# Kernel optimization log

Hardware: AMD Instinct MI355X
Metric: run time of the kernel (lower is better)

Reference implementation:

```python
import jax, jax.numpy as jnp
import numpy as np

N = 50000      # n_nodes
E = 1600000    # n_edges (avg degree 32)
IN = 512       # in_channels
H = 64         # hidden_channels
L = 32         # latent_channels


def _glorot(key, shape):
    lim = np.sqrt(6.0 / (shape[0] + shape[1])).astype(np.float32)
    return jax.random.uniform(key, shape, jnp.float32, -lim, lim)


def setup_inputs() -> dict:
    key = jax.random.key(0)
    ks = jax.random.split(key, 8)
    return {
        "x": jax.random.normal(ks[0], (N, IN), jnp.float32),
        "edge_index": jax.random.randint(ks[1], (2, E), 0, N, dtype=jnp.int64),
        "W1": _glorot(ks[2], (IN, H)), "b1": jnp.zeros((H,), jnp.float32),
        "W2": _glorot(ks[3], (H, L)), "b2": jnp.zeros((L,), jnp.float32),
        "Wd1": _glorot(ks[4], (L, H)), "bd1": jnp.zeros((H,), jnp.float32),
        "Wd2": _glorot(ks[5], (H, IN)), "bd2": jnp.zeros((IN,), jnp.float32),
    }


def reference(x, edge_index, W1, b1, W2, b2, Wd1, bd1, Wd2, bd2):
    n = x.shape[0]
    # GCNConv: add self-loops, symmetric normalization D^-1/2 (A+I) D^-1/2
    loops = jnp.arange(n, dtype=edge_index.dtype)
    src = jnp.concatenate([edge_index[0], loops])  # message sources
    dst = jnp.concatenate([edge_index[1], loops])  # aggregation targets
    deg = jax.ops.segment_sum(jnp.ones(src.shape[0], jnp.float32), dst,
                              num_segments=n)      # deg >= 1 (self-loop)
    dis = jax.lax.rsqrt(deg)                       # deg_inv_sqrt
    norm = dis[src] * dis[dst]                     # [E+N] edge coefficients

    def gcn_conv(h, W, b):
        hw = h @ W                                 # linear first (thin GEMM)
        msg = hw[src] * norm[:, None]              # gather + scale
        return jax.ops.segment_sum(msg, dst, num_segments=n) + b

    h = jax.nn.relu(gcn_conv(x, W1, b1))
    z = jax.nn.relu(gcn_conv(h, W2, b2))
    d = jax.nn.relu(z @ Wd1 + bd1)
    return jax.nn.sigmoid(d @ Wd2 + bd2)
```

## Files before the change

kernel.cpp:

```cpp
#include <hip/hip_runtime.h>

#define NN 50000
#define NE 1600000
#define CIN 512
#define CH 64
#define CL 32

#define SCAN_CHUNK 1024
#define NSCAN ((NN + SCAN_CHUNK - 1) / SCAN_CHUNK)

#define BKN 256
#define NB ((NN + BKN - 1) / BKN)
#define CHUNK 8192
#define NBLKA ((NE + CHUNK - 1) / CHUNK)
#define SEGCAP 12288

typedef float f32x4 __attribute__((ext_vector_type(4)));
typedef short bf16x8 __attribute__((ext_vector_type(8)));


__device__ inline unsigned short bf_hi(float f) {
    union { float f; unsigned u; } a; a.f = f;
    unsigned r = a.u + 0x7FFFu + ((a.u >> 16) & 1u);
    return (unsigned short)(r >> 16);
}
__device__ inline float bf_to_f(unsigned short h) {
    union { unsigned u; float f; } b; b.u = ((unsigned)h) << 16; return b.f;
}
__device__ inline void split_bf16(float f, unsigned short& hi, unsigned short& lo) {
    hi = bf_hi(f);
    lo = bf_hi(f - bf_to_f(hi));
}
__device__ inline void split4(const float4& v, ushort4& h, ushort4& l) {
    split_bf16(v.x, h.x, l.x); split_bf16(v.y, h.y, l.y);
    split_bf16(v.z, h.z, l.z); split_bf16(v.w, h.w, l.w);
}
__device__ inline void split8(const float4& v0, const float4& v1, bf16x8& h, bf16x8& l) {
    ushort4 h0, l0, h1, l1;
    split4(v0, h0, l0); split4(v1, h1, l1);
    h = (bf16x8){(short)h0.x, (short)h0.y, (short)h0.z, (short)h0.w,
                 (short)h1.x, (short)h1.y, (short)h1.z, (short)h1.w};
    l = (bf16x8){(short)l0.x, (short)l0.y, (short)l0.z, (short)l0.w,
                 (short)l1.x, (short)l1.y, (short)l1.z, (short)l1.w};
}

__device__ inline bf16x8 frag(const char* plane, int row, int koff_bytes) {
    int off = (row * 128 + koff_bytes) ^ ((row & 7) << 4);
    return *(const bf16x8*)(plane + off);
}


__global__ void k_prep(const float* __restrict__ W1, const float* __restrict__ Wd2,
                       unsigned short* __restrict__ wt1_hi, unsigned short* __restrict__ wt1_lo,
                       unsigned short* __restrict__ wt2_hi, unsigned short* __restrict__ wt2_lo) {
    int id = blockIdx.x * blockDim.x + threadIdx.x;
    if (id < CIN * CH) {
        int k = id >> 6, n = id & 63;
        unsigned short h, lo; split_bf16(W1[id], h, lo);
        wt1_hi[n * CIN + k] = h; wt1_lo[n * CIN + k] = lo;
    } else {
        int e = id - CIN * CH;
        int k = e >> 9, n = e & 511;
        unsigned short h, lo; split_bf16(Wd2[e], h, lo);
        wt2_hi[n * CH + k] = h; wt2_lo[n * CH + k] = lo;
    }
}


__global__ void k_init(int* cnt, int* gcur) {
    int i = blockIdx.x * blockDim.x + threadIdx.x;
    if (i < NN) cnt[i] = 0;
    if (i < NB) gcur[i] = 0;
}

__global__ void k_deg(const int* __restrict__ dst, int* __restrict__ cnt) {
    int e = blockIdx.x * blockDim.x + threadIdx.x;
    if (e < NE) atomicAdd(&cnt[dst[e]], 1);
}

__global__ void k_dis(const int* __restrict__ cnt, float* __restrict__ dis) {
    int i = blockIdx.x * blockDim.x + threadIdx.x;
    if (i < NN) dis[i] = rsqrtf((float)(cnt[i] + 1));
}

__global__ void k_scan_block(const int* __restrict__ cnt, int* __restrict__ rowptr,
                             int* __restrict__ bsum) {
    __shared__ int sd[256];
    int t = threadIdx.x, b = blockIdx.x;
    int base = b * SCAN_CHUNK + t * 4;
    int c[4], s = 0;
#pragma unroll
    for (int j = 0; j < 4; j++) {
        int i = base + j;
        c[j] = (i < NN) ? cnt[i] : 0;
        s += c[j];
    }
    sd[t] = s;
    __syncthreads();
    for (int off = 1; off < 256; off <<= 1) {
        int v = (t >= off) ? sd[t - off] : 0;
        __syncthreads();
        sd[t] += v;
        __syncthreads();
    }
    int incl = sd[t];
    int run = incl - s;
#pragma unroll
    for (int j = 0; j < 4; j++) {
        int i = base + j;
        if (i < NN) rowptr[i] = run;
        run += c[j];
    }
    if (t == 255) bsum[b] = incl;
}

__global__ void k_scan_top(int* bsum, int* rowptr) {
    int run = 0;
    for (int b = 0; b < NSCAN; b++) {
        int v = bsum[b];
        bsum[b] = run;
        run += v;
    }
    rowptr[NN] = run;
}

__global__ void k_scan_add(int* rowptr, const int* __restrict__ bsum) {
    int i = blockIdx.x * blockDim.x + threadIdx.x;
    if (i < NN) rowptr[i] += bsum[i >> 10];
}


__launch_bounds__(256)
__global__ void k_scatA(const int* __restrict__ srcIdx, const int* __restrict__ dstIdx,
                        const int* __restrict__ rowptr, int* __restrict__ gcur,
                        unsigned int* __restrict__ pairbuf) {
    __shared__ unsigned int stage[CHUNK];
    __shared__ unsigned char bids[CHUNK];
    __shared__ int hist[256], lbase[256], runcur[256], gbase[256];
    const int t = threadIdx.x;
    const int e0 = blockIdx.x * CHUNK;
    const int tot = min(NE - e0, CHUNK);

    hist[t] = 0; runcur[t] = 0;
    __syncthreads();

    unsigned int pr[CHUNK / 256];
    unsigned char bk[CHUNK / 256];
#pragma unroll
    for (int k = 0; k < CHUNK / 256; ++k) {
        int e = e0 + k * 256 + t;
        if (e < NE) {
            int s = srcIdx[e], d = dstIdx[e];
            pr[k] = ((unsigned)d << 16) | (unsigned)s;
            bk[k] = (unsigned char)(d >> 8);
            atomicAdd(&hist[bk[k]], 1);
        }
    }
    __syncthreads();
    int cb = hist[t];
    lbase[t] = cb;
    __syncthreads();
    for (int off = 1; off < 256; off <<= 1) {
        int v = (t >= off) ? lbase[t - off] : 0;
        __syncthreads();
        lbase[t] += v;
        __syncthreads();
    }
    int excl = lbase[t] - cb;
    __syncthreads();
    lbase[t] = excl;
    if (t < NB) {
        int base = rowptr[t * BKN];
        gbase[t] = base + (cb ? atomicAdd(&gcur[t], cb) : 0);
    }
    __syncthreads();
#pragma unroll
    for (int k = 0; k < CHUNK / 256; ++k) {
        int e = e0 + k * 256 + t;
        if (e < NE) {
            int b = bk[k];
            int off = lbase[b] + atomicAdd(&runcur[b], 1);
            stage[off] = pr[k];
            bids[off] = (unsigned char)b;
        }
    }
    __syncthreads();
    for (int i = t; i < tot; i += 256) {
        int b = bids[i];
        pairbuf[gbase[b] + (i - lbase[b])] = stage[i];
    }
}


__launch_bounds__(256)
__global__ void k_scatB(const int* __restrict__ rowptr, int* __restrict__ csr) {
    __shared__ int lcsr[SEGCAP];
    __shared__ int lrp[BKN + 1];
    __shared__ int lcur[BKN];
    const int t = threadIdx.x, b = blockIdx.x;
    const int n0 = b * BKN;
    const int nn = min(BKN, NN - n0);
    for (int i = t; i <= nn; i += 256) lrp[i] = rowptr[n0 + i];
    if (t < BKN) lcur[t] = 0;
    __syncthreads();
    const int p0 = lrp[0], p1 = lrp[nn];
    const int cnt = p1 - p0;
    for (int i = p0 + t; i < p1; i += 256) {
        unsigned int pr = ((const unsigned int*)csr)[i];
        int dL = (int)(pr >> 16) - n0;
        int slot = (lrp[dL] - p0) + atomicAdd(&lcur[dL], 1);
        lcsr[slot] = (int)(pr & 0xFFFFu);
    }
    __syncthreads();
    for (int i = t; i < cnt; i += 256) csr[p0 + i] = lcsr[i];
}


__launch_bounds__(256)
__global__ void k_gemm1_mfma(const float* __restrict__ x,
                             const unsigned short* __restrict__ wt_hi,
                             const unsigned short* __restrict__ wt_lo,
                             const float* __restrict__ dis,
                             float* __restrict__ hw1) {
    __shared__ alignas(16) char Ahi[8192], Alo[8192], Bhi[8192], Blo[8192];
    const int t = threadIdx.x;
    const int w = t >> 6, l = t & 63;
    const int row0 = blockIdx.x * 64;
    const int r = t >> 2;
    const int kq = (t & 3) * 16;

    f32x4 zero4 = {0.f, 0.f, 0.f, 0.f};
    f32x4 acc[4];
#pragma unroll
    for (int f = 0; f < 4; ++f) acc[f] = zero4;

    const bool inb = (row0 + r) < NN;

    for (int kc = 0; kc < CIN; kc += 64) {
        const float* xp = x + (row0 + r) * CIN + kc + kq;
#pragma unroll
        for (int j = 0; j < 4; ++j) {
            float4 v = inb ? *(const float4*)(xp + j * 4) : make_float4(0.f, 0.f, 0.f, 0.f);
            ushort4 h4, l4; split4(v, h4, l4);
            int so = (r * 128 + (kq + j * 4) * 2) ^ ((r & 7) << 4);
            *(ushort4*)(Ahi + so) = h4;
            *(ushort4*)(Alo + so) = l4;
        }
        {
            const char* bh = (const char*)wt_hi;
            const char* bl = (const char*)wt_lo;
            int kb = (t & 3) * 32;
#pragma unroll
            for (int j = 0; j < 2; ++j) {
                int srcoff = r * (CIN * 2) + kc * 2 + kb + j * 16;
                int so = (r * 128 + kb + j * 16) ^ ((r & 7) << 4);
                *(int4*)(Bhi + so) = *(const int4*)(bh + srcoff);
                *(int4*)(Blo + so) = *(const int4*)(bl + srcoff);
            }
        }
        __syncthreads();
#pragma unroll
        for (int ks = 0; ks < 2; ++ks) {
            int kb = ks * 64 + (l >> 4) * 16;
            bf16x8 aH = frag(Ahi, w * 16 + (l & 15), kb);
            bf16x8 aL = frag(Alo, w * 16 + (l & 15), kb);
#pragma unroll
            for (int f = 0; f < 4; ++f) {
                bf16x8 bH = frag(Bhi, f * 16 + (l & 15), kb);
                bf16x8 bL = frag(Blo, f * 16 + (l & 15), kb);
                acc[f] = __builtin_amdgcn_mfma_f32_16x16x32_bf16(aH, bH, acc[f], 0, 0, 0);
                acc[f] = __builtin_amdgcn_mfma_f32_16x16x32_bf16(aL, bH, acc[f], 0, 0, 0);
                acc[f] = __builtin_amdgcn_mfma_f32_16x16x32_bf16(aH, bL, acc[f], 0, 0, 0);
            }
        }
        __syncthreads();
    }
#pragma unroll
    for (int i = 0; i < 4; ++i) {
        int row = row0 + w * 16 + (l >> 4) * 4 + i;
        if (row < NN) {
            float di = dis[row];
#pragma unroll
            for (int f = 0; f < 4; ++f)
                hw1[row * CH + f * 16 + (l & 15)] = di * acc[f][i];
        }
    }
}


__launch_bounds__(256)
__global__ void k_agg1(const float* __restrict__ hw1s, const float* __restrict__ dis,
                       const int* __restrict__ rowptr, const int* __restrict__ csr,
                       const float* __restrict__ b1, float* __restrict__ h) {
    int i = blockIdx.x * 4 + (threadIdx.x >> 6);
    if (i >= NN) return;
    int c = threadIdx.x & 63;
    float a0 = hw1s[i * CH + c];
    float a1 = 0.f, a2 = 0.f, a3 = 0.f, a4 = 0.f, a5 = 0.f, a6 = 0.f, a7 = 0.f;
    int p = rowptr[i], p1 = rowptr[i + 1];
    for (; p + 8 <= p1; p += 8) {
        int s0 = csr[p + 0], s1 = csr[p + 1], s2 = csr[p + 2], s3 = csr[p + 3];
        int s4 = csr[p + 4], s5 = csr[p + 5], s6 = csr[p + 6], s7 = csr[p + 7];
        a0 += hw1s[s0 * CH + c]; a1 += hw1s[s1 * CH + c];
        a2 += hw1s[s2 * CH + c]; a3 += hw1s[s3 * CH + c];
        a4 += hw1s[s4 * CH + c]; a5 += hw1s[s5 * CH + c];
        a6 += hw1s[s6 * CH + c]; a7 += hw1s[s7 * CH + c];
    }
    for (; p < p1; ++p) a0 += hw1s[csr[p] * CH + c];
    float sum = ((a0 + a1) + (a2 + a3)) + ((a4 + a5) + (a6 + a7));
    float v = dis[i] * sum + b1[c];
    h[i * CH + c] = v > 0.f ? v : 0.f;
}


__global__ void k_gemm2(const float* __restrict__ h, const float* __restrict__ W2,
                        const float* __restrict__ dis, float* __restrict__ hz) {
    int t = blockIdx.x * blockDim.x + threadIdx.x;
    int n = t >> 5, c = t & 31;
    if (n >= NN) return;
    float acc = 0.f;
#pragma unroll
    for (int k = 0; k < CH; k++) acc = fmaf(h[n * CH + k], W2[k * CL + c], acc);
    hz[n * CL + c] = acc * dis[n];
}


__launch_bounds__(256)
__global__ void k_agg2(const float* __restrict__ hzs, const float* __restrict__ dis,
                       const int* __restrict__ rowptr, const int* __restrict__ csr,
                       const float* __restrict__ b2, float* __restrict__ z) {
    int wave = blockIdx.x * 4 + (threadIdx.x >> 6);
    int half = (threadIdx.x >> 5) & 1;
    int i = wave * 2 + half;
    if (i >= NN) return;
    int c = threadIdx.x & 31;
    float a0 = hzs[i * CL + c];
    float a1 = 0.f, a2 = 0.f, a3 = 0.f, a4 = 0.f, a5 = 0.f, a6 = 0.f, a7 = 0.f;
    int p = rowptr[i], p1 = rowptr[i + 1];
    for (; p + 8 <= p1; p += 8) {
        int s0 = csr[p + 0], s1 = csr[p + 1], s2 = csr[p + 2], s3 = csr[p + 3];
        int s4 = csr[p + 4], s5 = csr[p + 5], s6 = csr[p + 6], s7 = csr[p + 7];
        a0 += hzs[s0 * CL + c]; a1 += hzs[s1 * CL + c];
        a2 += hzs[s2 * CL + c]; a3 += hzs[s3 * CL + c];
        a4 += hzs[s4 * CL + c]; a5 += hzs[s5 * CL + c];
        a6 += hzs[s6 * CL + c]; a7 += hzs[s7 * CL + c];
    }
    for (; p < p1; ++p) a0 += hzs[csr[p] * CL + c];
    float sum = ((a0 + a1) + (a2 + a3)) + ((a4 + a5) + (a6 + a7));
    float v = dis[i] * sum + b2[c];
    z[i * CL + c] = v > 0.f ? v : 0.f;
}


__global__ void k_dmlp(const float* __restrict__ z, const float* __restrict__ Wd1,
                       const float* __restrict__ bd1, float* __restrict__ dout) {
    int g = blockIdx.x * blockDim.x + threadIdx.x;
    int n = g >> 6, c = g & 63;
    if (n >= NN) return;
    float acc = bd1[c];
    const float* zp = z + n * CL;
#pragma unroll
    for (int k = 0; k < CL; ++k) acc = fmaf(zp[k], Wd1[k * CH + c], acc);
    dout[n * CH + c] = acc > 0.f ? acc : 0.f;
}


__launch_bounds__(256)
__global__ void k_dec2(const float* __restrict__ d,
                       const unsigned short* __restrict__ wt2_hi,
                       const unsigned short* __restrict__ wt2_lo,
                       const float* __restrict__ bd2,
                       float* __restrict__ out) {
    __shared__ alignas(16) char Bh[16384], Bl[16384];
    const int t = threadIdx.x;
    const int w = t >> 6, l = t & 63;
    const int mt = blockIdx.x >> 2, nt = blockIdx.x & 3;
    const int row0 = mt * 64, col0 = nt * 128;
    const int lq = l >> 4, lr = l & 15;

    {
        int r = t >> 1, hf = (t & 1) * 64;
        const char* sh = (const char*)wt2_hi + (col0 + r) * 128 + hf;
        const char* sl = (const char*)wt2_lo + (col0 + r) * 128 + hf;
#pragma unroll
        for (int j = 0; j < 4; ++j) {
            int so = (r * 128 + hf + j * 16) ^ ((r & 7) << 4);
            *(int4*)(Bh + so) = *(const int4*)(sh + j * 16);
            *(int4*)(Bl + so) = *(const int4*)(sl + j * 16);
        }
    }

    const int arow = row0 + w * 16 + lr;
    const bool inb = arow < NN;
    bf16x8 aH[2], aL[2];
#pragma unroll
    for (int ks = 0; ks < 2; ++ks) {
        const float* ap = d + arow * CH + ks * 32 + lq * 8;
        float4 v0 = inb ? *(const float4*)ap : make_float4(0.f, 0.f, 0.f, 0.f);
        float4 v1 = inb ? *(const float4*)(ap + 4) : make_float4(0.f, 0.f, 0.f, 0.f);
        split8(v0, v1, aH[ks], aL[ks]);
    }
    __syncthreads();

    f32x4 zero4 = {0.f, 0.f, 0.f, 0.f};
    f32x4 acc[8];
#pragma unroll
    for (int f = 0; f < 8; ++f) acc[f] = zero4;

#pragma unroll
    for (int f = 0; f < 8; ++f) {
#pragma unroll
        for (int ks = 0; ks < 2; ++ks) {
            int kb = ks * 64 + lq * 16;
            bf16x8 bH = frag(Bh, f * 16 + lr, kb);
            bf16x8 bL = frag(Bl, f * 16 + lr, kb);
            acc[f] = __builtin_amdgcn_mfma_f32_16x16x32_bf16(aH[ks], bH, acc[f], 0, 0, 0);
            acc[f] = __builtin_amdgcn_mfma_f32_16x16x32_bf16(aL[ks], bH, acc[f], 0, 0, 0);
            acc[f] = __builtin_amdgcn_mfma_f32_16x16x32_bf16(aH[ks], bL, acc[f], 0, 0, 0);
        }
    }

#pragma unroll
    for (int f = 0; f < 8; ++f) {
        int c = col0 + f * 16 + lr;
        float bias = bd2[c];
#pragma unroll
        for (int i = 0; i < 4; ++i) {
            int row = row0 + w * 16 + lq * 4 + i;
            if (row < NN) {
                float v = acc[f][i] + bias;
                out[row * CIN + c] = 1.f / (1.f + __expf(-v));
            }
        }
    }
}


extern "C" void kernel_launch(void* const* d_in, const int* in_sizes, int n_in,
                              void* d_out, int out_size, void* d_ws, size_t ws_size,
                              hipStream_t stream) {
    const float* x   = (const float*)d_in[0];
    const int*   ei  = (const int*)d_in[1];
    const float* W1  = (const float*)d_in[2];
    const float* b1  = (const float*)d_in[3];
    const float* W2  = (const float*)d_in[4];
    const float* b2  = (const float*)d_in[5];
    const float* Wd1 = (const float*)d_in[6];
    const float* bd1 = (const float*)d_in[7];
    const float* Wd2 = (const float*)d_in[8];
    const float* bd2 = (const float*)d_in[9];
    const int* srcIdx = ei;
    const int* dstIdx = ei + NE;
    float* out = (float*)d_out;

    float* fws = (float*)d_ws;
    float* hw1 = fws;
    float* h   = hw1 + NN * CH;
    float* hz  = h + NN * CH;
    float* z   = hz + NN * CL;
    float* dis = z + NN * CL;
    int* cnt    = (int*)(dis + NN);
    int* rowptr = cnt + NN;
    int* gcur   = rowptr + NN + 1;
    int* bsum   = gcur + NB;
    int* csr    = bsum + 64;
    uintptr_t p = (uintptr_t)(csr + NE);
    p = (p + 63) & ~(uintptr_t)63;
    unsigned short* wt1_hi = (unsigned short*)p;
    unsigned short* wt1_lo = wt1_hi + CIN * CH;
    unsigned short* wt2_hi = wt1_lo + CIN * CH;
    unsigned short* wt2_lo = wt2_hi + CIN * CH;
    float* dbuf = hw1;

    const int nb_nodes = (NN + 255) / 256;
    const int nb_edges = (NE + 255) / 256;

    k_prep<<<256, 256, 0, stream>>>(W1, Wd2, wt1_hi, wt1_lo, wt2_hi, wt2_lo);

    k_init<<<nb_nodes, 256, 0, stream>>>(cnt, gcur);
    k_deg<<<nb_edges, 256, 0, stream>>>(dstIdx, cnt);
    k_dis<<<nb_nodes, 256, 0, stream>>>(cnt, dis);
    k_scan_block<<<NSCAN, 256, 0, stream>>>(cnt, rowptr, bsum);
    k_scan_top<<<1, 1, 0, stream>>>(bsum, rowptr);
    k_scan_add<<<nb_nodes, 256, 0, stream>>>(rowptr, bsum);
    k_scatA<<<NBLKA, 256, 0, stream>>>(srcIdx, dstIdx, rowptr, gcur, (unsigned int*)csr);
    k_scatB<<<NB, 256, 0, stream>>>(rowptr, csr);

    k_gemm1_mfma<<<(NN + 63) / 64, 256, 0, stream>>>(x, wt1_hi, wt1_lo, dis, hw1);
    k_agg1<<<(NN + 3) / 4, 256, 0, stream>>>(hw1, dis, rowptr, csr, b1, h);
    k_gemm2<<<(NN * 32 + 255) / 256, 256, 0, stream>>>(h, W2, dis, hz);
    k_agg2<<<(NN / 2 + 3) / 4, 256, 0, stream>>>(hz, dis, rowptr, csr, b2, z);
    k_dmlp<<<(NN * CH + 255) / 256, 256, 0, stream>>>(z, Wd1, bd1, dbuf);
    k_dec2<<<((NN + 63) / 64) * 4, 256, 0, stream>>>(dbuf, wt2_hi, wt2_lo, bd2, out);
}
```

Measured before the change: 492.7 us.

## Derive degrees and row pointers from bucketed scatter, dropping separate degree and scan passes

The separate degree-count atomics, node-level three-kernel scan and dis kernel are removed. The scatter pass now writes edges into fixed-capacity per-bucket segments of a scratch buffer (reusing the h buffer). A tiny bucket-level scan and the local CSR build then compute per-node counts, rowptr and dis inside shared memory. This removes one full pass over dst indices with global atomics plus several small launches. It relies on each 256-node bucket holding no more than SEGCAP edges, which holds for the uniform random test graph but could overflow on skewed graphs.

```diff
diff --git a/kernel.cpp b/kernel.cpp
--- a/kernel.cpp
+++ b/kernel.cpp
@@ -5,9 +5,6 @@
 #define CIN 512
 #define CH 64
 #define CL 32
-
-#define SCAN_CHUNK 1024
-#define NSCAN ((NN + SCAN_CHUNK - 1) / SCAN_CHUNK)
 
 #define BKN 256
 #define NB ((NN + BKN - 1) / BKN)
@@ -67,73 +64,15 @@
 }
 
 
-__global__ void k_init(int* cnt, int* gcur) {
+__global__ void k_init(int* gcur) {
     int i = blockIdx.x * blockDim.x + threadIdx.x;
-    if (i < NN) cnt[i] = 0;
     if (i < NB) gcur[i] = 0;
 }
 
-__global__ void k_deg(const int* __restrict__ dst, int* __restrict__ cnt) {
-    int e = blockIdx.x * blockDim.x + threadIdx.x;
-    if (e < NE) atomicAdd(&cnt[dst[e]], 1);
-}
-
-__global__ void k_dis(const int* __restrict__ cnt, float* __restrict__ dis) {
-    int i = blockIdx.x * blockDim.x + threadIdx.x;
-    if (i < NN) dis[i] = rsqrtf((float)(cnt[i] + 1));
-}
-
-__global__ void k_scan_block(const int* __restrict__ cnt, int* __restrict__ rowptr,
-                             int* __restrict__ bsum) {
-    __shared__ int sd[256];
-    int t = threadIdx.x, b = blockIdx.x;
-    int base = b * SCAN_CHUNK + t * 4;
-    int c[4], s = 0;
-#pragma unroll
-    for (int j = 0; j < 4; j++) {
-        int i = base + j;
-        c[j] = (i < NN) ? cnt[i] : 0;
-        s += c[j];
-    }
-    sd[t] = s;
-    __syncthreads();
-    for (int off = 1; off < 256; off <<= 1) {
-        int v = (t >= off) ? sd[t - off] : 0;
-        __syncthreads();
-        sd[t] += v;
-        __syncthreads();
-    }
-    int incl = sd[t];
-    int run = incl - s;
-#pragma unroll
-    for (int j = 0; j < 4; j++) {
-        int i = base + j;
-        if (i < NN) rowptr[i] = run;
-        run += c[j];
-    }
-    if (t == 255) bsum[b] = incl;
-}
-
-__global__ void k_scan_top(int* bsum, int* rowptr) {
-    int run = 0;
-    for (int b = 0; b < NSCAN; b++) {
-        int v = bsum[b];
-        bsum[b] = run;
-        run += v;
-    }
-    rowptr[NN] = run;
-}
-
-__global__ void k_scan_add(int* rowptr, const int* __restrict__ bsum) {
-    int i = blockIdx.x * blockDim.x + threadIdx.x;
-    if (i < NN) rowptr[i] += bsum[i >> 10];
-}
-
 
 __launch_bounds__(256)
 __global__ void k_scatA(const int* __restrict__ srcIdx, const int* __restrict__ dstIdx,
-                        const int* __restrict__ rowptr, int* __restrict__ gcur,
-                        unsigned int* __restrict__ pairbuf) {
+                        int* __restrict__ gcur, unsigned int* __restrict__ pairbuf) {
     __shared__ unsigned int stage[CHUNK];
     __shared__ unsigned char bids[CHUNK];
     __shared__ int hist[256], lbase[256], runcur[256], gbase[256];
@@ -170,8 +109,7 @@
     __syncthreads();
     lbase[t] = excl;
     if (t < NB) {
-        int base = rowptr[t * BKN];
-        gbase[t] = base + (cb ? atomicAdd(&gcur[t], cb) : 0);
+        gbase[t] = t * SEGCAP + (cb ? atomicAdd(&gcur[t], cb) : 0);
     }
     __syncthreads();
 #pragma unroll
@@ -191,28 +129,67 @@
     }
 }
 
-
-__launch_bounds__(256)
-__global__ void k_scatB(const int* __restrict__ rowptr, int* __restrict__ csr) {
+__global__ void k_bscan(const int* __restrict__ gcur, int* __restrict__ bbase,
+                        int* __restrict__ rowptr) {
+    __shared__ int sd[256];
+    int t = threadIdx.x;
+    int v = (t < NB) ? gcur[t] : 0;
+    sd[t] = v;
+    __syncthreads();
+    for (int off = 1; off < 256; off <<= 1) {
+        int u = (t >= off) ? sd[t - off] : 0;
+        __syncthreads();
+        sd[t] += u;
+        __syncthreads();
+    }
+    if (t < NB) bbase[t] = sd[t] - v;
+    if (t == 255) rowptr[NN] = sd[255];
+}
+
+
+__launch_bounds__(256)
+__global__ void k_scatB(const int* __restrict__ gcur, const int* __restrict__ bbase,
+                        const unsigned int* __restrict__ pairbuf,
+                        int* __restrict__ csr, int* __restrict__ rowptr,
+                        float* __restrict__ dis) {
     __shared__ int lcsr[SEGCAP];
-    __shared__ int lrp[BKN + 1];
-    __shared__ int lcur[BKN];
+    __shared__ int cntl[BKN], excl[BKN], lcur[BKN], sd[BKN];
     const int t = threadIdx.x, b = blockIdx.x;
     const int n0 = b * BKN;
-    const int nn = min(BKN, NN - n0);
-    for (int i = t; i <= nn; i += 256) lrp[i] = rowptr[n0 + i];
-    if (t < BKN) lcur[t] = 0;
-    __syncthreads();
-    const int p0 = lrp[0], p1 = lrp[nn];
-    const int cnt = p1 - p0;
-    for (int i = p0 + t; i < p1; i += 256) {
-        unsigned int pr = ((const unsigned int*)csr)[i];
+    const int m = gcur[b];
+    const int base = bbase[b];
+    const unsigned int* seg = pairbuf + b * SEGCAP;
+
+    cntl[t] = 0; lcur[t] = 0;
+    __syncthreads();
+    for (int i = t; i < m; i += 256)
+        atomicAdd(&cntl[(int)(seg[i] >> 16) - n0], 1);
+    __syncthreads();
+    int c = cntl[t];
+    sd[t] = c;
+    __syncthreads();
+    for (int off = 1; off < 256; off <<= 1) {
+        int u = (t >= off) ? sd[t - off] : 0;
+        __syncthreads();
+        sd[t] += u;
+        __syncthreads();
+    }
+    int ex = sd[t] - c;
+    excl[t] = ex;
+    int node = n0 + t;
+    if (node < NN) {
+        rowptr[node] = base + ex;
+        dis[node] = rsqrtf((float)(c + 1));
+    }
+    __syncthreads();
+    for (int i = t; i < m; i += 256) {
+        unsigned int pr = seg[i];
         int dL = (int)(pr >> 16) - n0;
-        int slot = (lrp[dL] - p0) + atomicAdd(&lcur[dL], 1);
+        int slot = excl[dL] + atomicAdd(&lcur[dL], 1);
         lcsr[slot] = (int)(pr & 0xFFFFu);
     }
     __syncthreads();
-    for (int i = t; i < cnt; i += 256) csr[p0 + i] = lcsr[i];
+    for (int i = t; i < m; i += 256) csr[base + i] = lcsr[i];
 }
 
 
@@ -459,32 +436,25 @@
     float* hz  = h + NN * CH;
     float* z   = hz + NN * CL;
     float* dis = z + NN * CL;
-    int* cnt    = (int*)(dis + NN);
-    int* rowptr = cnt + NN;
-    int* gcur   = rowptr + NN + 1;
-    int* bsum   = gcur + NB;
-    int* csr    = bsum + 64;
+    int* gcur   = (int*)(dis + NN);
+    int* bbase  = gcur + NB;
+    int* rowptr = bbase + NB;
+    int* csr    = rowptr + NN + 1;
     uintptr_t p = (uintptr_t)(csr + NE);
     p = (p + 63) & ~(uintptr_t)63;
     unsigned short* wt1_hi = (unsigned short*)p;
     unsigned short* wt1_lo = wt1_hi + CIN * CH;
     unsigned short* wt2_hi = wt1_lo + CIN * CH;
     unsigned short* wt2_lo = wt2_hi + CIN * CH;
+    unsigned int* pairbuf = (unsigned int*)h;
     float* dbuf = hw1;
 
-    const int nb_nodes = (NN + 255) / 256;
-    const int nb_edges = (NE + 255) / 256;
-
     k_prep<<<256, 256, 0, stream>>>(W1, Wd2, wt1_hi, wt1_lo, wt2_hi, wt2_lo);
 
-    k_init<<<nb_nodes, 256, 0, stream>>>(cnt, gcur);
-    k_deg<<<nb_edges, 256, 0, stream>>>(dstIdx, cnt);
-    k_dis<<<nb_nodes, 256, 0, stream>>>(cnt, dis);
-    k_scan_block<<<NSCAN, 256, 0, stream>>>(cnt, rowptr, bsum);
-    k_scan_top<<<1, 1, 0, stream>>>(bsum, rowptr);
-    k_scan_add<<<nb_nodes, 256, 0, stream>>>(rowptr, bsum);
-    k_scatA<<<NBLKA, 256, 0, stream>>>(srcIdx, dstIdx, rowptr, gcur, (unsigned int*)csr);
-    k_scatB<<<NB, 256, 0, stream>>>(rowptr, csr);
+    k_init<<<1, 256, 0, stream>>>(gcur);
+    k_scatA<<<NBLKA, 256, 0, stream>>>(srcIdx, dstIdx, gcur, pairbuf);
+    k_bscan<<<1, 256, 0, stream>>>(gcur, bbase, rowptr);
+    k_scatB<<<NB, 256, 0, stream>>>(gcur, bbase, pairbuf, csr, rowptr, dis);
 
     k_gemm1_mfma<<<(NN + 63) / 64, 256, 0, stream>>>(x, wt1_hi, wt1_lo, dis, hw1);
     k_agg1<<<(NN + 3) / 4, 256, 0, stream>>>(hw1, dis, rowptr, csr, b1, h);
```

After: 422.0 us. 1.17x faster.
